# Optimization experiments

Hardware: AMD Instinct MI355X
Metric: run time of the kernel (lower is better)

## Reference

```python
import jax, jax.numpy as jnp
import numpy as np

B = 2          # sequences
Q = 512        # queries per sequence (uniform; cu_seqlens_q is uniform)
HQ = 32        # query heads
HKV = 8        # kv heads (GQA)
D = 128        # head dim
BS = 128       # paged-cache block size
NBLK = 16      # blocks per sequence
MAXK = BS * NBLK   # 2048 max kv length
NUMBLOCKS = B * NBLK
WIN = 1024     # sliding window size
NEG = jnp.float32(-1e30)


def setup_inputs() -> dict:
    key = jax.random.key(0)
    k1, k2, k3 = jax.random.split(key, 3)
    q = jax.random.normal(k1, (B * Q, HQ, D), jnp.float32)
    # paged kv cache: [num_blocks, 2 (k/v), block_size, n_kv_heads, head_dim]
    ori_kv = jax.random.normal(k2, (NUMBLOCKS, 2, BS, HKV, D), jnp.float32)
    sinks = jax.random.normal(k3, (HQ,), jnp.float32)
    ori_block_table = jnp.arange(NUMBLOCKS, dtype=jnp.int32).reshape(B, NBLK)
    seqused_kv = jnp.array([2048, 1536], dtype=jnp.int32)  # per-seq used kv len (>= Q)
    mask = jnp.zeros((Q, MAXK), dtype=bool)  # extra user mask; True = masked out
    cu_seqlens_q = jnp.arange(B + 1, dtype=jnp.int32) * Q
    return {
        "q": q,
        "ori_block_table": ori_block_table,
        "ori_kv": ori_kv,
        "seqused_kv": seqused_kv,
        "sinks": sinks,
        "win_size": WIN,
        "mask": mask,
        "cu_seqlens_q": cu_seqlens_q,
    }


def reference(q, ori_block_table, ori_kv, seqused_kv, sinks, win_size, mask, cu_seqlens_q):
    # q: [B*Q, HQ, D] packed varlen (uniform Q per cu_seqlens_q)
    qb = q.reshape(B, Q, HQ, D)
    scale = 1.0 / jnp.sqrt(jnp.float32(D))

    # gather paged kv: [B, NBLK, 2, BS, HKV, D] -> [B, MAXK, 2, HKV, D]
    kv = ori_kv[ori_block_table]
    kv = kv.transpose(0, 1, 3, 2, 4, 5).reshape(B, MAXK, 2, HKV, D)
    k, v = kv[:, :, 0], kv[:, :, 1]             # [B, MAXK, HKV, D]
    rep = HQ // HKV
    k = jnp.repeat(k, rep, axis=2)               # [B, MAXK, HQ, D]
    v = jnp.repeat(v, rep, axis=2)

    # scores: [B, HQ, Q, MAXK]
    scores = jnp.einsum("bqhd,bkhd->bhqk", qb, k) * scale

    # causal + sliding-window + seq-length + user mask
    pos_q = seqused_kv[:, None] - Q + jnp.arange(Q)[None, :]       # [B, Q] absolute query pos
    j = jnp.arange(MAXK)                                           # key positions
    allow = (j[None, None, :] <= pos_q[:, :, None]) \
          & (j[None, None, :] > pos_q[:, :, None] - win_size) \
          & (j[None, None, :] < seqused_kv[:, None, None]) \
          & (~mask)[None, :, :]                                    # [B, Q, MAXK]
    scores = jnp.where(allow[:, None, :, :], scores, NEG)

    # softmax with attention sink: sink logit joins the denominator only
    m = jnp.maximum(scores.max(axis=-1), sinks[None, :, None])     # [B, HQ, Q]
    p = jnp.exp(scores - m[..., None])                             # [B, HQ, Q, MAXK]
    denom = p.sum(axis=-1) + jnp.exp(sinks[None, :, None] - m)     # [B, HQ, Q]

    out = jnp.einsum("bhqk,bkhd->bqhd", p, v) / denom.transpose(0, 2, 1)[..., None]
    return out.reshape(B * Q, HQ, D)
```

## Files before the change

### kernel.cpp

```cpp
#include <hip/hip_runtime.h>
#include <hip/hip_bf16.h>


#define B_    2
#define Q_    512
#define HQ_   32
#define HKV_  8
#define D_    128
#define BS_   128
#define NBLK_ 16
#define QBLK  64
#define KBLK  64
#define PP    72
#define KVROW (HKV_*D_)

typedef __attribute__((ext_vector_type(8))) __bf16 bf16x8;
typedef __attribute__((ext_vector_type(4))) float  f32x4;
typedef __attribute__((ext_vector_type(4))) float  float4v;
typedef __attribute__((ext_vector_type(4))) unsigned int u32x4;
typedef __attribute__((ext_vector_type(2))) unsigned int u32x2;

#if __has_builtin(__builtin_amdgcn_exp2f)
#define EXP2(x) __builtin_amdgcn_exp2f(x)
#else
#define EXP2(x) exp2f(x)
#endif

__device__ __forceinline__ unsigned pk2(float a, float b) {
    union { __bf16 h[2]; unsigned u; } x;
    x.h[0] = (__bf16)a; x.h[1] = (__bf16)b;
    return x.u;
}

__global__ __launch_bounds__(256, 2) void swa_kernel(
    const float* __restrict__ q,
    const int*   __restrict__ btab,
    const float* __restrict__ kv,
    const int*   __restrict__ seqused,
    const float* __restrict__ sinks,
    const int*   __restrict__ winp,
    float*       __restrict__ out)
{
    __shared__ __align__(16) unsigned short Klds[64 * 128];
    __shared__ __align__(16) unsigned short Vlds[64 * 128];
    __shared__ __align__(16) unsigned short Plds[4][16 * PP];

    const int tid  = threadIdx.x;
    const int lane = tid & 63;
    const int w    = tid >> 6;
    const int l15  = lane & 15;
    const int lhi  = lane >> 4;

    const int bid = blockIdx.x;
    const int qt  = bid & 7;
    const int h   = (bid >> 3) & 31;
    const int b   = bid >> 8;
    const int kh  = h >> 2;

    const int seq  = seqused[b];
    const int win  = winp[0];
    const int q0   = qt * QBLK;
    const int pos0 = seq - Q_ + q0;

    const int lo  = pos0 - win + 1;
    const int jt0 = (lo < 0 ? 0 : lo) & ~63;
    const int jt1 = (pos0 + QBLK - 1) & ~63;

    const float SCL2 = 0.08838834764831845f * 1.4426950408889634f;

    const int    qr    = q0 + w * 16 + l15;
    const size_t qbase = ((size_t)(b * Q_ + qr) * HQ_ + h) * D_;
    bf16x8 qf[4];
    #pragma unroll
    for (int dc = 0; dc < 4; ++dc) {
        const float4v f0 = *reinterpret_cast<const float4v*>(q + qbase + dc * 32 + lhi * 8);
        const float4v f1 = *reinterpret_cast<const float4v*>(q + qbase + dc * 32 + lhi * 8 + 4);
        u32x4 p;
        p[0] = pk2(f0[0] * SCL2, f0[1] * SCL2); p[1] = pk2(f0[2] * SCL2, f0[3] * SCL2);
        p[2] = pk2(f1[0] * SCL2, f1[1] * SCL2); p[3] = pk2(f1[2] * SCL2, f1[3] * SCL2);
        qf[dc] = __builtin_bit_cast(bf16x8, p);
    }

    const int   pqmin = pos0 + w * 16;
    const int   pqmax = pqmin + 15;
    const int   posq  = pqmin + l15;
    const float sink2 = sinks[h] * 1.4426950408889634f;
    float mrun = sink2;
    float lrun = 1.0f;
    f32x4 o[8];
    #pragma unroll
    for (int g = 0; g < 8; ++g) o[g] = (f32x4){0.f, 0.f, 0.f, 0.f};

    for (int jt = jt0; jt <= jt1; jt += KBLK) {
        const int    blk    = btab[b * NBLK_ + (jt >> 7)];
        const size_t kgbase = (size_t)blk * (2 * BS_ * KVROW) + (size_t)(jt & 127) * KVROW + kh * D_;
        const size_t vgbase = kgbase + (size_t)BS_ * KVROW;

        __syncthreads();

        {
            const int kl = tid >> 2;
            const int cb = (tid & 3) * 64;
            const float* src = kv + kgbase + (size_t)kl * KVROW + (tid & 3) * 32;
            char* dst = (char*)Klds + kl * 256;
            #pragma unroll
            for (int i = 0; i < 4; ++i) {
                const float4v f0 = *reinterpret_cast<const float4v*>(src + i * 8);
                const float4v f1 = *reinterpret_cast<const float4v*>(src + i * 8 + 4);
                u32x4 p;
                p[0] = pk2(f0[0], f0[1]); p[1] = pk2(f0[2], f0[3]);
                p[2] = pk2(f1[0], f1[1]); p[3] = pk2(f1[2], f1[3]);
                *reinterpret_cast<u32x4*>(dst + ((cb + i * 16) ^ ((kl & 15) << 4))) = p;
            }
        }
        {
            const int db = tid & 31;
            #pragma unroll
            for (int half = 0; half < 2; ++half) {
                const int kb = (tid >> 5) + half * 8;
                const int k0 = kb * 4;
                const float* vsrc = kv + vgbase + (size_t)k0 * KVROW + db * 4;
                const float4v r0 = *reinterpret_cast<const float4v*>(vsrc);
                const float4v r1 = *reinterpret_cast<const float4v*>(vsrc + KVROW);
                const float4v r2 = *reinterpret_cast<const float4v*>(vsrc + 2 * KVROW);
                const float4v r3 = *reinterpret_cast<const float4v*>(vsrc + 3 * KVROW);
                #pragma unroll
                for (int dd = 0; dd < 4; ++dd) {
                    const int d    = db * 4 + dd;
                    const int g    = d >> 4;
                    const int slot = ((kb >> 1) & 3) * 16 + ((d & 15) ^ (g & 7));
                    const int elem = (g * 2 + (k0 >> 5)) * 512 + slot * 8 + (k0 & 7);
                    u32x2 wv;
                    wv[0] = pk2(r0[dd], r1[dd]);
                    wv[1] = pk2(r2[dd], r3[dd]);
                    *reinterpret_cast<u32x2*>(&Vlds[elem]) = wv;
                }
            }
        }
        __syncthreads();

        if (jt > pqmax || jt + KBLK - 1 <= pqmin - win) continue;
        const bool edge = (jt + KBLK - 1 > pqmin) || (jt <= pqmax - win);

        f32x4 sacc[4];
        #pragma unroll
        for (int g = 0; g < 4; ++g) sacc[g] = (f32x4){0.f, 0.f, 0.f, 0.f};
        #pragma unroll
        for (int g = 0; g < 4; ++g) {
            const char* krow = (const char*)Klds + (g * 16 + l15) * 256;
            const int   swz  = (l15 << 4);
            #pragma unroll
            for (int dc = 0; dc < 4; ++dc) {
                const bf16x8 a = *reinterpret_cast<const bf16x8*>(
                    krow + ((dc * 64 + lhi * 16) ^ swz));
                sacc[g] = __builtin_amdgcn_mfma_f32_16x16x32_bf16(a, qf[dc], sacc[g], 0, 0, 0);
            }
        }

        float sv[16];
        float mloc = -3e38f;
        if (edge) {
            #pragma unroll
            for (int g = 0; g < 4; ++g) {
                #pragma unroll
                for (int i = 0; i < 4; ++i) {
                    const int  kglob = jt + g * 16 + lhi * 4 + i;
                    const bool ok = (kglob <= posq) && (kglob > posq - win);
                    const float s = ok ? sacc[g][i] : -1e30f;
                    sv[g * 4 + i] = s;
                    mloc = fmaxf(mloc, s);
                }
            }
        } else {
            #pragma unroll
            for (int g = 0; g < 4; ++g) {
                #pragma unroll
                for (int i = 0; i < 4; ++i) {
                    sv[g * 4 + i] = sacc[g][i];
                    mloc = fmaxf(mloc, sacc[g][i]);
                }
            }
        }
        mloc = fmaxf(mloc, __shfl_xor(mloc, 16));
        mloc = fmaxf(mloc, __shfl_xor(mloc, 32));

        if (!__all(mloc <= mrun + 8.0f)) {
            const float mnew  = fmaxf(mrun, mloc);
            const float alpha = EXP2(mrun - mnew);
            lrun *= alpha;
            #pragma unroll
            for (int g = 0; g < 8; ++g) o[g] *= alpha;
            mrun = mnew;
        }

        float ps = 0.f;
        unsigned pw[8];
        #pragma unroll
        for (int t = 0; t < 8; ++t) {
            const float p0 = EXP2(sv[2 * t]     - mrun);
            const float p1 = EXP2(sv[2 * t + 1] - mrun);
            ps += p0 + p1;
            pw[t] = pk2(p0, p1);
        }
        ps += __shfl_xor(ps, 16);
        ps += __shfl_xor(ps, 32);
        lrun += ps;

        #pragma unroll
        for (int g = 0; g < 4; ++g) {
            u32x2 wv; wv[0] = pw[2 * g]; wv[1] = pw[2 * g + 1];
            *reinterpret_cast<u32x2*>(&Plds[w][l15 * PP + g * 16 + lhi * 4]) = wv;
        }

        #pragma unroll
        for (int kc = 0; kc < 2; ++kc) {
            const bf16x8 pf = *reinterpret_cast<const bf16x8*>(
                &Plds[w][l15 * PP + kc * 32 + lhi * 8]);
            #pragma unroll
            for (int g = 0; g < 8; ++g) {
                const bf16x8 vf = *reinterpret_cast<const bf16x8*>(
                    &Vlds[(g * 2 + kc) * 512 + (lhi * 16 + (l15 ^ (g & 7))) * 8]);
                o[g] = __builtin_amdgcn_mfma_f32_16x16x32_bf16(vf, pf, o[g], 0, 0, 0);
            }
        }
    }

    const float  inv   = 1.0f / lrun;
    const size_t obase = ((size_t)(b * Q_ + qr) * HQ_ + h) * D_;
    #pragma unroll
    for (int g = 0; g < 8; ++g) {
        float4v v;
        v[0] = o[g][0] * inv; v[1] = o[g][1] * inv;
        v[2] = o[g][2] * inv; v[3] = o[g][3] * inv;
        *reinterpret_cast<float4v*>(out + obase + g * 16 + lhi * 4) = v;
    }
}

extern "C" void kernel_launch(void* const* d_in, const int* in_sizes, int n_in,
                              void* d_out, int out_size, void* d_ws, size_t ws_size,
                              hipStream_t stream) {
    const float* q       = (const float*)d_in[0];
    const int*   btab    = (const int*)  d_in[1];
    const float* kv      = (const float*)d_in[2];
    const int*   seqused = (const int*)  d_in[3];
    const float* sinks   = (const float*)d_in[4];
    const int*   win     = (const int*)  d_in[5];
    float* out = (float*)d_out;

    swa_kernel<<<dim3(B_ * HQ_ * (Q_ / QBLK)), dim3(256), 0, stream>>>(
        q, btab, kv, seqused, sinks, win, out);
}
```

Measured before the change: 64.27 us.

## Pre-convert KV cache to swizzled bf16 workspace and double-buffer async LDS loads

Adds a prepass kernel that converts the fp32 paged KV cache once into bf16 tiles already swizzled for LDS, K row-major and V transposed. The main kernel then streams these tiles with global_load_lds into double-buffered shared memory, prefetching the next tile while computing the current one. The goal is to remove the per-block fp32 to bf16 conversion and repacking, which the many query blocks sharing each KV head currently repeat, and to halve global read bytes in the main loop. In exchange there is an extra kernel launch plus a workspace write and read, and twice the LDS per block, which may limit occupancy. The old kernel is kept as a fallback for when the workspace is too small.

```diff
diff --git a/kernel.cpp b/kernel.cpp
--- a/kernel.cpp
+++ b/kernel.cpp
@@ -9,6 +9,7 @@
 #define D_    128
 #define BS_   128
 #define NBLK_ 16
+#define NPHYS (B_*NBLK_)
 #define QBLK  64
 #define KBLK  64
 #define PP    72
@@ -32,7 +33,264 @@
     return x.u;
 }
 
-__global__ __launch_bounds__(256, 2) void swa_kernel(
+__device__ __forceinline__ void gld16(const void* g, void* l) {
+    __builtin_amdgcn_global_load_lds(
+        (const __attribute__((address_space(1))) void*)g,
+        (__attribute__((address_space(3))) void*)l, 16, 0, 0);
+}
+
+__global__ __launch_bounds__(256) void swa_prepass(
+    const float* __restrict__ kv,
+    unsigned short* __restrict__ wsK,
+    unsigned short* __restrict__ wsV)
+{
+    const int tid  = threadIdx.x;
+    const int pk   = blockIdx.x >> 1;
+    const int part = blockIdx.x & 1;
+    const int phys = pk >> 3;
+    const int kh   = pk & 7;
+
+    if (part == 0) {
+        const int row = tid >> 1;
+        const int dh  = (tid & 1) * 64;
+        const float* src = kv + ((size_t)(phys * 2 + 0) * BS_ + row) * KVROW + kh * D_ + dh;
+        char* dstrow = (char*)(wsK + ((size_t)pk * BS_ + row) * D_);
+        const int swz = (row & 15) << 4;
+        #pragma unroll
+        for (int i = 0; i < 8; ++i) {
+            const float4v f0 = *reinterpret_cast<const float4v*>(src + i * 8);
+            const float4v f1 = *reinterpret_cast<const float4v*>(src + i * 8 + 4);
+            u32x4 p;
+            p[0] = pk2(f0[0], f0[1]); p[1] = pk2(f0[2], f0[3]);
+            p[2] = pk2(f1[0], f1[1]); p[3] = pk2(f1[2], f1[3]);
+            *reinterpret_cast<u32x4*>(dstrow + ((dh * 2 + i * 16) ^ swz)) = p;
+        }
+    } else {
+        const int db  = tid & 31;
+        const int kb8 = tid >> 5;
+        #pragma unroll
+        for (int tile = 0; tile < 2; ++tile) {
+            unsigned short* dstt = wsV + ((size_t)pk * 2 + tile) * 8192;
+            #pragma unroll
+            for (int half = 0; half < 2; ++half) {
+                const int kb  = kb8 + half * 8;
+                const int k0  = kb * 4;
+                const int key = tile * 64 + k0;
+                const float* vsrc = kv + ((size_t)(phys * 2 + 1) * BS_ + key) * KVROW + kh * D_ + db * 4;
+                const float4v r0 = *reinterpret_cast<const float4v*>(vsrc);
+                const float4v r1 = *reinterpret_cast<const float4v*>(vsrc + KVROW);
+                const float4v r2 = *reinterpret_cast<const float4v*>(vsrc + 2 * KVROW);
+                const float4v r3 = *reinterpret_cast<const float4v*>(vsrc + 3 * KVROW);
+                #pragma unroll
+                for (int dd = 0; dd < 4; ++dd) {
+                    const int d    = db * 4 + dd;
+                    const int g    = d >> 4;
+                    const int slot = ((kb >> 1) & 3) * 16 + ((d & 15) ^ (g & 7));
+                    const int elem = (g * 2 + (k0 >> 5)) * 512 + slot * 8 + (k0 & 7);
+                    u32x2 wv;
+                    wv[0] = pk2(r0[dd], r1[dd]);
+                    wv[1] = pk2(r2[dd], r3[dd]);
+                    *reinterpret_cast<u32x2*>(dstt + elem) = wv;
+                }
+            }
+        }
+    }
+}
+
+__global__ __launch_bounds__(256, 2) void swa_main(
+    const float* __restrict__ q,
+    const int*   __restrict__ btab,
+    const int*   __restrict__ seqused,
+    const float* __restrict__ sinks,
+    const int*   __restrict__ winp,
+    const unsigned short* __restrict__ wsK,
+    const unsigned short* __restrict__ wsV,
+    float*       __restrict__ out)
+{
+    __shared__ __align__(16) unsigned short Kb[2][8192];
+    __shared__ __align__(16) unsigned short Vb[2][8192];
+    __shared__ __align__(16) unsigned short Pl[4][16 * PP];
+
+    const int tid  = threadIdx.x;
+    const int lane = tid & 63;
+    const int w    = tid >> 6;
+    const int l15  = lane & 15;
+    const int lhi  = lane >> 4;
+
+    const int bid = blockIdx.x;
+    const int qt  = bid & 7;
+    const int h   = (bid >> 3) & 31;
+    const int b   = bid >> 8;
+    const int kh  = h >> 2;
+
+    const int seq  = seqused[b];
+    const int win  = winp[0];
+    const int q0   = qt * QBLK;
+    const int pos0 = seq - Q_ + q0;
+
+    const int lo  = pos0 - win + 1;
+    const int jt0 = (lo < 0 ? 0 : lo) & ~63;
+    const int jt1 = (pos0 + QBLK - 1) & ~63;
+    const int nt  = ((jt1 - jt0) >> 6) + 1;
+
+    const float SCL2 = 0.08838834764831845f * 1.4426950408889634f;
+
+    const int    qr    = q0 + w * 16 + l15;
+    const size_t qbase = ((size_t)(b * Q_ + qr) * HQ_ + h) * D_;
+    bf16x8 qf[4];
+    #pragma unroll
+    for (int dc = 0; dc < 4; ++dc) {
+        const float4v f0 = *reinterpret_cast<const float4v*>(q + qbase + dc * 32 + lhi * 8);
+        const float4v f1 = *reinterpret_cast<const float4v*>(q + qbase + dc * 32 + lhi * 8 + 4);
+        u32x4 p;
+        p[0] = pk2(f0[0] * SCL2, f0[1] * SCL2); p[1] = pk2(f0[2] * SCL2, f0[3] * SCL2);
+        p[2] = pk2(f1[0] * SCL2, f1[1] * SCL2); p[3] = pk2(f1[2] * SCL2, f1[3] * SCL2);
+        qf[dc] = __builtin_bit_cast(bf16x8, p);
+    }
+
+    const int   pqmin = pos0 + w * 16;
+    const int   pqmax = pqmin + 15;
+    const int   posq  = pqmin + l15;
+    const float sink2 = sinks[h] * 1.4426950408889634f;
+    float mrun = sink2;
+    float lrun = 1.0f;
+    f32x4 o[8];
+    #pragma unroll
+    for (int g = 0; g < 8; ++g) o[g] = (f32x4){0.f, 0.f, 0.f, 0.f};
+
+    {
+        const int blk = btab[b * NBLK_ + (jt0 >> 7)];
+        const unsigned short* ks = wsK + ((size_t)(blk * 8 + kh) * BS_ + (jt0 & 127)) * D_;
+        const unsigned short* vs = wsV + ((size_t)(blk * 8 + kh) * 2 + ((jt0 >> 6) & 1)) * 8192;
+        #pragma unroll
+        for (int i = 0; i < 4; ++i)
+            gld16(ks + (w * 4 + i) * 512 + lane * 8, &Kb[0][(w * 4 + i) * 512]);
+        #pragma unroll
+        for (int i = 0; i < 4; ++i)
+            gld16(vs + (w * 4 + i) * 512 + lane * 8, &Vb[0][(w * 4 + i) * 512]);
+    }
+    __syncthreads();
+
+    int cur = 0;
+    for (int t = 0; t < nt; ++t) {
+        const int jt = jt0 + t * KBLK;
+
+        if (t + 1 < nt) {
+            const int jn  = jt + KBLK;
+            const int blk = btab[b * NBLK_ + (jn >> 7)];
+            const unsigned short* ks = wsK + ((size_t)(blk * 8 + kh) * BS_ + (jn & 127)) * D_;
+            const unsigned short* vs = wsV + ((size_t)(blk * 8 + kh) * 2 + ((jn >> 6) & 1)) * 8192;
+            const int nb = cur ^ 1;
+            #pragma unroll
+            for (int i = 0; i < 4; ++i)
+                gld16(ks + (w * 4 + i) * 512 + lane * 8, &Kb[nb][(w * 4 + i) * 512]);
+            #pragma unroll
+            for (int i = 0; i < 4; ++i)
+                gld16(vs + (w * 4 + i) * 512 + lane * 8, &Vb[nb][(w * 4 + i) * 512]);
+        }
+
+        if (jt <= pqmax && jt + KBLK - 1 > pqmin - win) {
+            const bool edge = (jt + KBLK - 1 > pqmin) || (jt <= pqmax - win);
+
+            f32x4 sacc[4];
+            #pragma unroll
+            for (int g = 0; g < 4; ++g) sacc[g] = (f32x4){0.f, 0.f, 0.f, 0.f};
+            #pragma unroll
+            for (int g = 0; g < 4; ++g) {
+                const char* krow = (const char*)&Kb[cur][0] + (g * 16 + l15) * 256;
+                const int   swz  = (l15 << 4);
+                #pragma unroll
+                for (int dc = 0; dc < 4; ++dc) {
+                    const bf16x8 a = *reinterpret_cast<const bf16x8*>(
+                        krow + ((dc * 64 + lhi * 16) ^ swz));
+                    sacc[g] = __builtin_amdgcn_mfma_f32_16x16x32_bf16(a, qf[dc], sacc[g], 0, 0, 0);
+                }
+            }
+
+            float sv[16];
+            float mloc = -3e38f;
+            if (edge) {
+                #pragma unroll
+                for (int g = 0; g < 4; ++g) {
+                    #pragma unroll
+                    for (int i = 0; i < 4; ++i) {
+                        const int  kglob = jt + g * 16 + lhi * 4 + i;
+                        const bool ok = (kglob <= posq) && (kglob > posq - win);
+                        const float s = ok ? sacc[g][i] : -1e30f;
+                        sv[g * 4 + i] = s;
+                        mloc = fmaxf(mloc, s);
+                    }
+                }
+            } else {
+                #pragma unroll
+                for (int g = 0; g < 4; ++g) {
+                    #pragma unroll
+                    for (int i = 0; i < 4; ++i) {
+                        sv[g * 4 + i] = sacc[g][i];
+                        mloc = fmaxf(mloc, sacc[g][i]);
+                    }
+                }
+            }
+            mloc = fmaxf(mloc, __shfl_xor(mloc, 16));
+            mloc = fmaxf(mloc, __shfl_xor(mloc, 32));
+
+            if (!__all(mloc <= mrun + 8.0f)) {
+                const float mnew  = fmaxf(mrun, mloc);
+                const float alpha = EXP2(mrun - mnew);
+                lrun *= alpha;
+                #pragma unroll
+                for (int g = 0; g < 8; ++g) o[g] *= alpha;
+                mrun = mnew;
+            }
+
+            float ps = 0.f;
+            unsigned pw[8];
+            #pragma unroll
+            for (int t2 = 0; t2 < 8; ++t2) {
+                const float p0 = EXP2(sv[2 * t2]     - mrun);
+                const float p1 = EXP2(sv[2 * t2 + 1] - mrun);
+                ps += p0 + p1;
+                pw[t2] = pk2(p0, p1);
+            }
+            ps += __shfl_xor(ps, 16);
+            ps += __shfl_xor(ps, 32);
+            lrun += ps;
+
+            #pragma unroll
+            for (int g = 0; g < 4; ++g) {
+                u32x2 wv; wv[0] = pw[2 * g]; wv[1] = pw[2 * g + 1];
+                *reinterpret_cast<u32x2*>(&Pl[w][l15 * PP + g * 16 + lhi * 4]) = wv;
+            }
+
+            #pragma unroll
+            for (int kc = 0; kc < 2; ++kc) {
+                const bf16x8 pf = *reinterpret_cast<const bf16x8*>(
+                    &Pl[w][l15 * PP + kc * 32 + lhi * 8]);
+                #pragma unroll
+                for (int g = 0; g < 8; ++g) {
+                    const bf16x8 vf = *reinterpret_cast<const bf16x8*>(
+                        &Vb[cur][(g * 2 + kc) * 512 + (lhi * 16 + (l15 ^ (g & 7))) * 8]);
+                    o[g] = __builtin_amdgcn_mfma_f32_16x16x32_bf16(vf, pf, o[g], 0, 0, 0);
+                }
+            }
+        }
+
+        __syncthreads();
+        cur ^= 1;
+    }
+
+    const float  inv   = 1.0f / lrun;
+    const size_t obase = ((size_t)(b * Q_ + qr) * HQ_ + h) * D_;
+    #pragma unroll
+    for (int g = 0; g < 8; ++g) {
+        float4v v;
+        v[0] = o[g][0] * inv; v[1] = o[g][1] * inv;
+        v[2] = o[g][2] * inv; v[3] = o[g][3] * inv;
+        *reinterpret_cast<float4v*>(out + obase + g * 16 + lhi * 4) = v;
+    }
+}
+
+__global__ __launch_bounds__(256, 2) void swa_fallback(
     const float* __restrict__ q,
     const int*   __restrict__ btab,
     const float* __restrict__ kv,
@@ -97,7 +355,6 @@
         const size_t vgbase = kgbase + (size_t)BS_ * KVROW;
 
         __syncthreads();
-
         {
             const int kl = tid >> 2;
             const int cb = (tid & 3) * 64;
@@ -247,6 +504,18 @@
     const int*   win     = (const int*)  d_in[5];
     float* out = (float*)d_out;
 
-    swa_kernel<<<dim3(B_ * HQ_ * (Q_ / QBLK)), dim3(256), 0, stream>>>(
-        q, btab, kv, seqused, sinks, win, out);
+    const size_t wsK_elems = (size_t)NPHYS * 8 * BS_ * D_;
+    const size_t wsV_elems = (size_t)NPHYS * 8 * 2 * 8192;
+    const size_t need_bytes = (wsK_elems + wsV_elems) * 2;
+
+    if (ws_size >= need_bytes) {
+        unsigned short* wsK = (unsigned short*)d_ws;
+        unsigned short* wsV = wsK + wsK_elems;
+        swa_prepass<<<dim3(NPHYS * 8 * 2), dim3(256), 0, stream>>>(kv, wsK, wsV);
+        swa_main<<<dim3(B_ * HQ_ * (Q_ / QBLK)), dim3(256), 0, stream>>>(
+            q, btab, seqused, sinks, win, wsK, wsV, out);
+    } else {
+        swa_fallback<<<dim3(B_ * HQ_ * (Q_ / QBLK)), dim3(256), 0, stream>>>(
+            q, btab, kv, seqused, sinks, win, out);
+    }
 }
```

Result: faster. 55.86 us (-13.1%).
